# Kernel optimization log

Hardware: AMD Instinct MI355X
Metric: run time of the kernel (lower is better)

Reference implementation:

```python
import jax, jax.numpy as jnp
import numpy as np

N_HEADS = 16


def setup_inputs() -> dict:
    key = jax.random.key(0)
    k_x, k_len, k_pos, k_attn, k_proj = jax.random.split(key, 5)
    B, W, c, C = 4, 256, 32, 1024
    x = jax.random.normal(k_x, (B, W, c, C), dtype=jnp.float32)
    # ragged word lengths in [1, c]; left-aligned padding mask as in pad()
    lengths = jax.random.randint(k_len, (B, W), 1, c + 1)
    attention_mask = (jnp.arange(c)[None, None, :] < lengths[:, :, None]).astype(jnp.int32)
    pos_emb = jax.random.normal(k_pos, (W, C), dtype=jnp.float32) * 0.02
    attn_w = jax.random.normal(k_attn, (C, 3 * C), dtype=jnp.float32) * (C ** -0.5)
    proj_w = jax.random.normal(k_proj, (C, C), dtype=jnp.float32) * (C ** -0.5)
    return {"x": x, "attention_mask": attention_mask, "pos_emb": pos_emb,
            "attn_w": attn_w, "proj_w": proj_w}


def reference(x, attention_mask, pos_emb, attn_w, proj_w):
    # first_time=True path of CharAttention.forward (eval mode: dropout = identity)
    B, W, c, C = x.shape
    H = N_HEADS
    hd = C // H
    last_ix = jnp.sum(attention_mask, axis=2) - 1          # [B, W]

    qkv = jnp.einsum('bwce,ef->bwcf', x, attn_w)            # [B, W, c, 3C]
    q, k, v = jnp.split(qkv, 3, axis=-1)
    # [B, W, c, C] -> [B, W, H, c, hd]
    def to_heads(t):
        return t.reshape(B, W, c, H, hd).transpose(0, 1, 3, 2, 4)
    q, k, v = to_heads(q), to_heads(k), to_heads(v)

    scale = 1.0 / jnp.sqrt(jnp.asarray(hd, dtype=x.dtype))
    scores = jnp.einsum('bwhqd,bwhkd->bwhqk', q, k) * scale  # [B, W, H, c, c]
    causal = jnp.tril(jnp.ones((c, c), dtype=bool))
    scores = jnp.where(causal[None, None, None], scores, jnp.finfo(x.dtype).min)
    attn = jax.nn.softmax(scores, axis=-1)
    o = jnp.einsum('bwhqk,bwhkd->bwhqd', attn, v)            # [B, W, H, c, hd]
    o = o.transpose(0, 1, 3, 2, 4).reshape(B, W, c, C)       # [B, W, c, C]

    # gather the last real-character position of each word
    idx = last_ix[:, :, None, None]                          # [B, W, 1, 1]
    gathered = jnp.take_along_axis(o, idx, axis=2)[:, :, 0, :]  # [B, W, C]

    out = gathered + pos_emb[None, :, :]
    out = jnp.einsum('bwe,ef->bwf', out, proj_w)
    return out
```

## Files before the change

kernel.cpp:

```cpp
#include <hip/hip_runtime.h>
#include <hip/hip_bf16.h>
#include <stdint.h>

typedef __attribute__((ext_vector_type(8))) short short8;
typedef __attribute__((ext_vector_type(4))) float floatx4;

#define GPTR(p) (const __attribute__((address_space(1))) void*)(p)
#define LPTR(p) (__attribute__((address_space(3))) void*)(p)

__device__ __forceinline__ ushort f2bf(float f) {
    union { float f; uint32_t u; } v; v.f = f;
    uint32_t u = v.u;
    uint32_t r = (u + 0x7FFFu + ((u >> 16) & 1u)) >> 16;
    return (ushort)r;
}
__device__ __forceinline__ float bf2f(ushort b) {
    union { uint32_t u; float f; } v; v.u = ((uint32_t)b) << 16;
    return v.f;
}

__global__ void prep_kernel(const float* __restrict__ attn_w, const float* __restrict__ proj_w,
                            const float* __restrict__ x, const int* __restrict__ mask,
                            ushort* __restrict__ wqT, ushort* __restrict__ wk,
                            ushort* __restrict__ wvT, ushort* __restrict__ wpT,
                            ushort* __restrict__ xq) {
    __shared__ float tile[32][33];
    __shared__ int t_sh;
    const int bx = blockIdx.x, by = blockIdx.y;
    const int tid = threadIdx.x;

    if (bx >= 128) {
        int bw = (bx - 128) * 32 + by;
        if (tid < 32) {
            int s = mask[bw * 32 + tid];
            #pragma unroll
            for (int off = 16; off; off >>= 1) s += __shfl_xor(s, off);
            if (tid == 0) t_sh = s - 1;
        }
        __syncthreads();
        int t = t_sh;
        float4 v = ((const float4*)(x + ((size_t)bw * 32 + t) * 1024))[tid];
        ushort4 o;
        o.x = f2bf(v.x); o.y = f2bf(v.y); o.z = f2bf(v.z); o.w = f2bf(v.w);
        ((ushort4*)(xq + (size_t)bw * 1024))[tid] = o;
        return;
    }

    const int tx = tid & 31, ty = tid >> 5;
    const int r0 = by * 32;
    if (bx >= 96) {
        int c0 = (bx - 96) * 32;
        for (int i = ty; i < 32; i += 8)
            wk[(size_t)(r0 + i) * 1024 + c0 + tx] =
                f2bf(attn_w[(size_t)(r0 + i) * 3072 + 1024 + c0 + tx]);
        return;
    }
    const float* src; ushort* dst; int N, csrc0, c0;
    if (bx < 32)      { src = attn_w; dst = wqT; N = 3072; c0 = bx * 32;        csrc0 = c0; }
    else if (bx < 64) { src = attn_w; dst = wvT; N = 3072; c0 = (bx - 32) * 32; csrc0 = 2048 + c0; }
    else              { src = proj_w; dst = wpT; N = 1024; c0 = (bx - 64) * 32; csrc0 = c0; }
    for (int i = ty; i < 32; i += 8)
        tile[i][tx] = src[(size_t)(r0 + i) * N + csrc0 + tx];
    __syncthreads();
    for (int i = ty; i < 32; i += 8)
        dst[(size_t)(c0 + i) * 1024 + r0 + tx] = f2bf(tile[tx][i]);
}

template <bool OUT_BF16, bool ADD_POS>
__global__ __launch_bounds__(256)
void gemm64db_kernel(const ushort* __restrict__ A, int lda, long sA,
                     const ushort* __restrict__ Bt, int ldb, long sB,
                     void* __restrict__ C, int ldc, int cColPerZ, int K,
                     const float* __restrict__ pos) {
    __shared__ ushort As[2][64 * 32];
    __shared__ ushort Bs[2][64 * 32];

    const int bm = blockIdx.x, bn = blockIdx.y, z = blockIdx.z;
    A  += (size_t)z * sA;
    Bt += (size_t)z * sB;

    const int tid  = threadIdx.x;
    const int wave = tid >> 6;
    const int lane = tid & 63;
    const int wm = wave & 1, wn = wave >> 1;
    const int quad = lane >> 4, l15 = lane & 15;

    floatx4 acc[2][2] = {};

    const int srow = wave * 16 + (lane >> 2);
    const int kcol = (lane & 3) * 8;
    const ushort* gA = A  + (size_t)(bm * 64 + srow) * lda + kcol;
    const ushort* gB = Bt + (size_t)(bn * 64 + srow) * ldb + kcol;
    const int lofs = wave * 512;

    __builtin_amdgcn_global_load_lds(GPTR(gA), LPTR(As[0] + lofs), 16, 0, 0);
    __builtin_amdgcn_global_load_lds(GPTR(gB), LPTR(Bs[0] + lofs), 16, 0, 0);
    __syncthreads();

    int cur = 0;
    for (int kt = 0; kt < K; kt += 32) {
        if (kt + 32 < K) {
            __builtin_amdgcn_global_load_lds(GPTR(gA + kt + 32), LPTR(As[cur ^ 1] + lofs), 16, 0, 0);
            __builtin_amdgcn_global_load_lds(GPTR(gB + kt + 32), LPTR(Bs[cur ^ 1] + lofs), 16, 0, 0);
        }
        short8 af[2], bf[2];
        #pragma unroll
        for (int i = 0; i < 2; ++i)
            af[i] = *(const short8*)&As[cur][(wm * 32 + i * 16 + l15) * 32 + quad * 8];
        #pragma unroll
        for (int j = 0; j < 2; ++j)
            bf[j] = *(const short8*)&Bs[cur][(wn * 32 + j * 16 + l15) * 32 + quad * 8];
        #pragma unroll
        for (int i = 0; i < 2; ++i)
            #pragma unroll
            for (int j = 0; j < 2; ++j)
                acc[i][j] = __builtin_amdgcn_mfma_f32_16x16x32_bf16(af[i], bf[j], acc[i][j], 0, 0, 0);
        __syncthreads();
        cur ^= 1;
    }

    #pragma unroll
    for (int i = 0; i < 2; ++i) {
        #pragma unroll
        for (int j = 0; j < 2; ++j) {
            int r0 = bm * 64 + wm * 32 + i * 16 + quad * 4;
            int cc = z * cColPerZ + bn * 64 + wn * 32 + j * 16 + l15;
            #pragma unroll
            for (int r = 0; r < 4; ++r) {
                float v = acc[i][j][r];
                if (ADD_POS) v += pos[(size_t)((r0 + r) & 255) * 1024 + cc];
                size_t idx = (size_t)(r0 + r) * ldc + cc;
                if (OUT_BF16) ((ushort*)C)[idx] = f2bf(v);
                else          ((float*) C)[idx] = v;
            }
        }
    }
}

__global__ __launch_bounds__(256)
void gemmu_kernel(const ushort* __restrict__ A, const ushort* __restrict__ Bt,
                  ushort* __restrict__ C) {
    const int bm = blockIdx.x, bn = blockIdx.y, z = blockIdx.z;
    const int tid  = threadIdx.x;
    const int wave = tid >> 6;
    const int lane = tid & 63;
    const int wm = wave & 1, wn = wave >> 1;
    const int quad = lane >> 4, l15 = lane & 15;

    const ushort* Ab = A  + (size_t)(bm * 128 + wm * 64 + l15) * 1024 + z * 64 + quad * 8;
    const ushort* Bb = Bt + (size_t)(bn * 128 + wn * 64 + l15) * 1024 + z * 64 + quad * 8;

    short8 af[4][2], bfr[4][2];
    #pragma unroll
    for (int i = 0; i < 4; ++i)
        #pragma unroll
        for (int kk = 0; kk < 2; ++kk) {
            af[i][kk]  = *(const short8*)(Ab + (size_t)(i * 16) * 1024 + kk * 32);
            bfr[i][kk] = *(const short8*)(Bb + (size_t)(i * 16) * 1024 + kk * 32);
        }

    floatx4 acc[4][4] = {};
    #pragma unroll
    for (int kk = 0; kk < 2; ++kk)
        #pragma unroll
        for (int i = 0; i < 4; ++i)
            #pragma unroll
            for (int j = 0; j < 4; ++j)
                acc[i][j] = __builtin_amdgcn_mfma_f32_16x16x32_bf16(af[i][kk], bfr[j][kk], acc[i][j], 0, 0, 0);

    #pragma unroll
    for (int i = 0; i < 4; ++i) {
        #pragma unroll
        for (int j = 0; j < 4; ++j) {
            int r0 = bm * 128 + wm * 64 + i * 16 + quad * 4;
            int c  = bn * 128 + wn * 64 + j * 16 + l15;
            #pragma unroll
            for (int r = 0; r < 4; ++r)
                C[(size_t)(r0 + r) * 16384 + (size_t)z * 1024 + c] = f2bf(acc[i][j][r]);
        }
    }
}

__global__ __launch_bounds__(256)
void attn2_kernel(const float* __restrict__ x, const int* __restrict__ mask,
                  const ushort* __restrict__ U, ushort* __restrict__ Z) {
    __shared__ float  Sp[2][16][16];
    __shared__ float  Ss[16 * 36];
    __shared__ float  Ps[32 * 16];
    __shared__ int    t_sh;

    const int bw = blockIdx.x;
    const int tid = threadIdx.x;
    const int wave = tid >> 6, lane = tid & 63;
    const int quad = lane >> 4, l15 = lane & 15;

    if (tid < 32) {
        int s = mask[bw * 32 + tid];
        #pragma unroll
        for (int off = 16; off; off >>= 1) s += __shfl_xor(s, off);
        if (tid == 0) t_sh = s - 1;
    }
    __syncthreads();
    const int t = t_sh;

    const int m  = wave & 1;
    const int kh = wave >> 1;
    const int row = m * 16 + l15;
    const bool live = (row <= t);

    const float*  xrow = x + ((size_t)bw * 32 + row) * 1024 + kh * 512 + quad * 8;
    const ushort* urow = U + (size_t)bw * 16384 + (size_t)l15 * 1024 + kh * 512 + quad * 8;

    floatx4 acc = {0.f, 0.f, 0.f, 0.f};
    #pragma unroll
    for (int ks = 0; ks < 16; ++ks) {
        short8 a = (short8)0;
        if (live) {
            float4 v0 = *(const float4*)(xrow + ks * 32);
            float4 v1 = *(const float4*)(xrow + ks * 32 + 4);
            a[0] = (short)f2bf(v0.x); a[1] = (short)f2bf(v0.y);
            a[2] = (short)f2bf(v0.z); a[3] = (short)f2bf(v0.w);
            a[4] = (short)f2bf(v1.x); a[5] = (short)f2bf(v1.y);
            a[6] = (short)f2bf(v1.z); a[7] = (short)f2bf(v1.w);
        }
        short8 b = *(const short8*)(urow + ks * 32);
        acc = __builtin_amdgcn_mfma_f32_16x16x32_bf16(a, b, acc, 0, 0, 0);
    }

    if (kh == 1) {
        #pragma unroll
        for (int r = 0; r < 4; ++r) Sp[m][quad * 4 + r][l15] = acc[r];
    }
    __syncthreads();
    if (kh == 0) {
        #pragma unroll
        for (int r = 0; r < 4; ++r)
            Ss[l15 * 36 + m * 16 + quad * 4 + r] =
                (acc[r] + Sp[m][quad * 4 + r][l15]) * 0.125f;
    }
    __syncthreads();

    if (wave == 0) {
        float s[8]; float mx = -1e30f;
        #pragma unroll
        for (int r = 0; r < 8; ++r) {
            int j = quad * 8 + r;
            float v = Ss[l15 * 36 + j];
            v = (j <= t) ? v : -1e30f;
            s[r] = v; mx = fmaxf(mx, v);
        }
        mx = fmaxf(mx, __shfl_xor(mx, 16));
        mx = fmaxf(mx, __shfl_xor(mx, 32));
        float l = 0.f;
        #pragma unroll
        for (int r = 0; r < 8; ++r) { s[r] = __expf(s[r] - mx); l += s[r]; }
        l += __shfl_xor(l, 16);
        l += __shfl_xor(l, 32);
        float inv = 1.f / l;
        #pragma unroll
        for (int r = 0; r < 8; ++r)
            Ps[(quad * 8 + r) * 16 + l15] = s[r] * inv;
    }
    __syncthreads();

    const float4* xsrc = (const float4*)(x + (size_t)bw * 32768);
    float z[16][4];
    #pragma unroll
    for (int h = 0; h < 16; ++h)
        #pragma unroll
        for (int cc = 0; cc < 4; ++cc) z[h][cc] = 0.f;
    for (int j = 0; j <= t; ++j) {
        float4 p0 = *(const float4*)&Ps[j * 16 + 0];
        float4 p1 = *(const float4*)&Ps[j * 16 + 4];
        float4 p2 = *(const float4*)&Ps[j * 16 + 8];
        float4 p3 = *(const float4*)&Ps[j * 16 + 12];
        float pr[16] = {p0.x, p0.y, p0.z, p0.w, p1.x, p1.y, p1.z, p1.w,
                        p2.x, p2.y, p2.z, p2.w, p3.x, p3.y, p3.z, p3.w};
        float4 xv = xsrc[j * 256 + tid];
        float xf[4] = {xv.x, xv.y, xv.z, xv.w};
        #pragma unroll
        for (int h = 0; h < 16; ++h)
            #pragma unroll
            for (int cc = 0; cc < 4; ++cc)
                z[h][cc] += pr[h] * xf[cc];
    }
    const int e0 = tid * 4;
    #pragma unroll
    for (int h = 0; h < 16; ++h) {
        ushort4 o;
        o.x = f2bf(z[h][0]); o.y = f2bf(z[h][1]);
        o.z = f2bf(z[h][2]); o.w = f2bf(z[h][3]);
        *(ushort4*)&Z[(size_t)bw * 16384 + h * 1024 + e0] = o;
    }
}

extern "C" void kernel_launch(void* const* d_in, const int* in_sizes, int n_in,
                              void* d_out, int out_size, void* d_ws, size_t ws_size,
                              hipStream_t stream) {
    const float* x        = (const float*)d_in[0];
    const int*   mask     = (const int*)  d_in[1];
    const float* pos_emb  = (const float*)d_in[2];
    const float* attn_w   = (const float*)d_in[3];
    const float* proj_w   = (const float*)d_in[4];
    float*       out      = (float*)d_out;

    const long MB2 = 1048576;

    char* ws = (char*)d_ws;
    size_t off = 0;
    ushort* U_bf  = (ushort*)(ws + off); off += (size_t)16 * MB2 * 2;
    ushort* Z_bf  = (ushort*)(ws + off); off += (size_t)16 * MB2 * 2;
    ushort* wqT   = (ushort*)(ws + off); off += MB2 * 2;
    ushort* wk    = (ushort*)(ws + off); off += MB2 * 2;
    ushort* wvT   = (ushort*)(ws + off); off += MB2 * 2;
    ushort* wpT   = (ushort*)(ws + off); off += MB2 * 2;
    ushort* xq_bf = (ushort*)(ws + off); off += MB2 * 2;
    ushort* q_bf  = (ushort*)(ws + off); off += MB2 * 2;
    ushort* y_bf  = (ushort*)(ws + off); off += MB2 * 2;

    prep_kernel<<<dim3(160, 32), 256, 0, stream>>>(attn_w, proj_w, x, mask,
                                                   wqT, wk, wvT, wpT, xq_bf);

    gemm64db_kernel<true, false><<<dim3(16, 16, 1), 256, 0, stream>>>(
        xq_bf, 1024, 0, wqT, 1024, 0, (void*)q_bf, 1024, 0, 1024, nullptr);

    gemmu_kernel<<<dim3(8, 8, 16), 256, 0, stream>>>(q_bf, wk, U_bf);

    attn2_kernel<<<1024, 256, 0, stream>>>(x, mask, U_bf, Z_bf);

    gemm64db_kernel<true, true><<<dim3(16, 1, 16), 256, 0, stream>>>(
        Z_bf, 16384, 1024, wvT, 1024, 65536, (void*)y_bf, 1024, 64, 1024, pos_emb);

    gemm64db_kernel<false, false><<<dim3(16, 16, 1), 256, 0, stream>>>(
        y_bf, 1024, 0, wpT, 1024, 0, (void*)out, 1024, 0, 1024, nullptr);
}
```

Measured before the change: 277.8 us.

## Fuse all six stage kernels into one persistent kernel with grid barriers

Replaces the six separate launches (weight prep, q GEMM, U GEMM, attention, V GEMM, proj GEMM) with one persistent kernel of 512 blocks. The blocks loop over each stage's tiles and meet at an atomic-based grid barrier between stages. The aim is to remove per-launch overhead and the idle gaps between dependent kernels. In exchange, the barrier has a timeout break that could silently let blocks proceed early. It also depends on all 512 blocks being co-resident (launch bounds of 2 blocks per CU), and the fixed grid may balance uneven stages worse than the original launches.

```diff
diff --git a/kernel.cpp b/kernel.cpp
--- a/kernel.cpp
+++ b/kernel.cpp
@@ -14,19 +14,37 @@
     uint32_t r = (u + 0x7FFFu + ((u >> 16) & 1u)) >> 16;
     return (ushort)r;
 }
-__device__ __forceinline__ float bf2f(ushort b) {
-    union { uint32_t u; float f; } v; v.u = ((uint32_t)b) << 16;
-    return v.f;
-}
-
-__global__ void prep_kernel(const float* __restrict__ attn_w, const float* __restrict__ proj_w,
+
+__device__ int g_bar_count;
+__device__ int g_bar_gen;
+
+__device__ __forceinline__ void grid_sync(int nb) {
+    __syncthreads();
+    if (threadIdx.x == 0) {
+        int g = __hip_atomic_load(&g_bar_gen, __ATOMIC_RELAXED, __HIP_MEMORY_SCOPE_AGENT);
+        int prev = __hip_atomic_fetch_add(&g_bar_count, 1, __ATOMIC_ACQ_REL, __HIP_MEMORY_SCOPE_AGENT);
+        if (prev == nb - 1) {
+            __hip_atomic_store(&g_bar_count, 0, __ATOMIC_RELAXED, __HIP_MEMORY_SCOPE_AGENT);
+            __hip_atomic_store(&g_bar_gen, g + 1, __ATOMIC_RELEASE, __HIP_MEMORY_SCOPE_AGENT);
+        } else {
+            long long t0 = clock64();
+            while (__hip_atomic_load(&g_bar_gen, __ATOMIC_ACQUIRE, __HIP_MEMORY_SCOPE_AGENT) == g) {
+                __builtin_amdgcn_s_sleep(8);
+                if (clock64() - t0 > 100000000LL) break;
+            }
+        }
+    }
+    __syncthreads();
+}
+
+__device__ __forceinline__ void prep_body(int bx, int by,
+                            const float* __restrict__ attn_w, const float* __restrict__ proj_w,
                             const float* __restrict__ x, const int* __restrict__ mask,
                             ushort* __restrict__ wqT, ushort* __restrict__ wk,
                             ushort* __restrict__ wvT, ushort* __restrict__ wpT,
                             ushort* __restrict__ xq) {
     __shared__ float tile[32][33];
-    __shared__ int t_sh;
-    const int bx = blockIdx.x, by = blockIdx.y;
+    __shared__ int t_sh0;
     const int tid = threadIdx.x;
 
     if (bx >= 128) {
@@ -35,14 +53,15 @@
             int s = mask[bw * 32 + tid];
             #pragma unroll
             for (int off = 16; off; off >>= 1) s += __shfl_xor(s, off);
-            if (tid == 0) t_sh = s - 1;
+            if (tid == 0) t_sh0 = s - 1;
         }
         __syncthreads();
-        int t = t_sh;
+        int t = t_sh0;
         float4 v = ((const float4*)(x + ((size_t)bw * 32 + t) * 1024))[tid];
         ushort4 o;
         o.x = f2bf(v.x); o.y = f2bf(v.y); o.z = f2bf(v.z); o.w = f2bf(v.w);
         ((ushort4*)(xq + (size_t)bw * 1024))[tid] = o;
+        __syncthreads();
         return;
     }
 
@@ -64,18 +83,17 @@
     __syncthreads();
     for (int i = ty; i < 32; i += 8)
         dst[(size_t)(c0 + i) * 1024 + r0 + tx] = f2bf(tile[tx][i]);
+    __syncthreads();
 }
 
 template <bool OUT_BF16, bool ADD_POS>
-__global__ __launch_bounds__(256)
-void gemm64db_kernel(const ushort* __restrict__ A, int lda, long sA,
+__device__ __forceinline__ void gemm_body(const ushort* __restrict__ A, int lda, long sA,
                      const ushort* __restrict__ Bt, int ldb, long sB,
                      void* __restrict__ C, int ldc, int cColPerZ, int K,
-                     const float* __restrict__ pos) {
+                     const float* __restrict__ pos, int bm, int bn, int z) {
     __shared__ ushort As[2][64 * 32];
     __shared__ ushort Bs[2][64 * 32];
 
-    const int bm = blockIdx.x, bn = blockIdx.y, z = blockIdx.z;
     A  += (size_t)z * sA;
     Bt += (size_t)z * sB;
 
@@ -137,10 +155,8 @@
     }
 }
 
-__global__ __launch_bounds__(256)
-void gemmu_kernel(const ushort* __restrict__ A, const ushort* __restrict__ Bt,
-                  ushort* __restrict__ C) {
-    const int bm = blockIdx.x, bn = blockIdx.y, z = blockIdx.z;
+__device__ __forceinline__ void gemmu_body(const ushort* __restrict__ A, const ushort* __restrict__ Bt,
+                  ushort* __restrict__ C, int bm, int bn, int z) {
     const int tid  = threadIdx.x;
     const int wave = tid >> 6;
     const int lane = tid & 63;
@@ -181,15 +197,13 @@
     }
 }
 
-__global__ __launch_bounds__(256)
-void attn2_kernel(const float* __restrict__ x, const int* __restrict__ mask,
-                  const ushort* __restrict__ U, ushort* __restrict__ Z) {
+__device__ __forceinline__ void attn2_body(const float* __restrict__ x, const int* __restrict__ mask,
+                  const ushort* __restrict__ U, ushort* __restrict__ Zo, int bw) {
     __shared__ float  Sp[2][16][16];
     __shared__ float  Ss[16 * 36];
     __shared__ float  Ps[32 * 16];
     __shared__ int    t_sh;
 
-    const int bw = blockIdx.x;
     const int tid = threadIdx.x;
     const int wave = tid >> 6, lane = tid & 63;
     const int quad = lane >> 4, l15 = lane & 15;
@@ -264,11 +278,11 @@
     __syncthreads();
 
     const float4* xsrc = (const float4*)(x + (size_t)bw * 32768);
-    float z[16][4];
+    float zz[16][4];
     #pragma unroll
     for (int h = 0; h < 16; ++h)
         #pragma unroll
-        for (int cc = 0; cc < 4; ++cc) z[h][cc] = 0.f;
+        for (int cc = 0; cc < 4; ++cc) zz[h][cc] = 0.f;
     for (int j = 0; j <= t; ++j) {
         float4 p0 = *(const float4*)&Ps[j * 16 + 0];
         float4 p1 = *(const float4*)&Ps[j * 16 + 4];
@@ -282,16 +296,54 @@
         for (int h = 0; h < 16; ++h)
             #pragma unroll
             for (int cc = 0; cc < 4; ++cc)
-                z[h][cc] += pr[h] * xf[cc];
+                zz[h][cc] += pr[h] * xf[cc];
     }
     const int e0 = tid * 4;
     #pragma unroll
     for (int h = 0; h < 16; ++h) {
         ushort4 o;
-        o.x = f2bf(z[h][0]); o.y = f2bf(z[h][1]);
-        o.z = f2bf(z[h][2]); o.w = f2bf(z[h][3]);
-        *(ushort4*)&Z[(size_t)bw * 16384 + h * 1024 + e0] = o;
-    }
+        o.x = f2bf(zz[h][0]); o.y = f2bf(zz[h][1]);
+        o.z = f2bf(zz[h][2]); o.w = f2bf(zz[h][3]);
+        *(ushort4*)&Zo[(size_t)bw * 16384 + h * 1024 + e0] = o;
+    }
+}
+
+__global__ __launch_bounds__(256, 2)
+void mega_kernel(const float* __restrict__ x, const int* __restrict__ mask,
+                 const float* __restrict__ pos, const float* __restrict__ attn_w,
+                 const float* __restrict__ proj_w, float* __restrict__ out,
+                 ushort* __restrict__ U, ushort* __restrict__ Z,
+                 ushort* __restrict__ wqT, ushort* __restrict__ wk,
+                 ushort* __restrict__ wvT, ushort* __restrict__ wpT,
+                 ushort* __restrict__ xq, ushort* __restrict__ q,
+                 ushort* __restrict__ y) {
+    const int nb = gridDim.x;
+
+    for (int task = blockIdx.x; task < 5120; task += nb)
+        prep_body(task % 160, task / 160, attn_w, proj_w, x, mask, wqT, wk, wvT, wpT, xq);
+    grid_sync(nb);
+
+    for (int task = blockIdx.x; task < 256; task += nb)
+        gemm_body<true, false>(xq, 1024, 0, wqT, 1024, 0, (void*)q, 1024, 0, 1024,
+                               nullptr, task & 15, task >> 4, 0);
+    grid_sync(nb);
+
+    for (int task = blockIdx.x; task < 1024; task += nb)
+        gemmu_body(q, wk, U, task & 7, (task >> 3) & 7, task >> 6);
+    grid_sync(nb);
+
+    for (int task = blockIdx.x; task < 1024; task += nb)
+        attn2_body(x, mask, U, Z, task);
+    grid_sync(nb);
+
+    for (int task = blockIdx.x; task < 256; task += nb)
+        gemm_body<true, true>(Z, 16384, 1024, wvT, 1024, 65536, (void*)y, 1024, 64, 1024,
+                              pos, task & 15, 0, task >> 4);
+    grid_sync(nb);
+
+    for (int task = blockIdx.x; task < 256; task += nb)
+        gemm_body<false, false>(y, 1024, 0, wpT, 1024, 0, (void*)out, 1024, 0, 1024,
+                                nullptr, task & 15, task >> 4, 0);
 }
 
 extern "C" void kernel_launch(void* const* d_in, const int* in_sizes, int n_in,
@@ -318,19 +370,7 @@
     ushort* q_bf  = (ushort*)(ws + off); off += MB2 * 2;
     ushort* y_bf  = (ushort*)(ws + off); off += MB2 * 2;
 
-    prep_kernel<<<dim3(160, 32), 256, 0, stream>>>(attn_w, proj_w, x, mask,
-                                                   wqT, wk, wvT, wpT, xq_bf);
-
-    gemm64db_kernel<true, false><<<dim3(16, 16, 1), 256, 0, stream>>>(
-        xq_bf, 1024, 0, wqT, 1024, 0, (void*)q_bf, 1024, 0, 1024, nullptr);
-
-    gemmu_kernel<<<dim3(8, 8, 16), 256, 0, stream>>>(q_bf, wk, U_bf);
-
-    attn2_kernel<<<1024, 256, 0, stream>>>(x, mask, U_bf, Z_bf);
-
-    gemm64db_kernel<true, true><<<dim3(16, 1, 16), 256, 0, stream>>>(
-        Z_bf, 16384, 1024, wvT, 1024, 65536, (void*)y_bf, 1024, 64, 1024, pos_emb);
-
-    gemm64db_kernel<false, false><<<dim3(16, 16, 1), 256, 0, stream>>>(
-        y_bf, 1024, 0, wpT, 1024, 0, (void*)out, 1024, 0, 1024, nullptr);
-}
+    mega_kernel<<<dim3(512), dim3(256), 0, stream>>>(
+        x, mask, pos_emb, attn_w, proj_w, out,
+        U_bf, Z_bf, wqT, wk, wvT, wpT, xq_bf, q_bf, y_bf);
+}
```

Result: slower. 789.8 us (+184.3%).

## Split K across two wave groups in small GEMMs with LDS reduction

Applied to the files above, without the earlier changes.

The 64x64-tile GEMM kernel now runs 8 waves per block, with two groups of four waves each handling half of the K dimension in separate double-buffered LDS slices. After the loop, the second group writes its partial accumulators to a shared float buffer and the first group adds them before the epilogue. This doubles waves per block for these small-grid GEMMs (256 blocks) to hide latency and halves the serial K loop. The cost is extra LDS use, one extra reduction pass and a barrier.

```diff
diff --git a/kernel.cpp b/kernel.cpp
--- a/kernel.cpp
+++ b/kernel.cpp
@@ -13,10 +13,6 @@
     uint32_t u = v.u;
     uint32_t r = (u + 0x7FFFu + ((u >> 16) & 1u)) >> 16;
     return (ushort)r;
-}
-__device__ __forceinline__ float bf2f(ushort b) {
-    union { uint32_t u; float f; } v; v.u = ((uint32_t)b) << 16;
-    return v.f;
 }
 
 __global__ void prep_kernel(const float* __restrict__ attn_w, const float* __restrict__ proj_w,
@@ -67,49 +63,55 @@
 }
 
 template <bool OUT_BF16, bool ADD_POS>
-__global__ __launch_bounds__(256)
-void gemm64db_kernel(const ushort* __restrict__ A, int lda, long sA,
+__global__ __launch_bounds__(512)
+void gemm64x8_kernel(const ushort* __restrict__ A, int lda, long sA,
                      const ushort* __restrict__ Bt, int ldb, long sB,
                      void* __restrict__ C, int ldc, int cColPerZ, int K,
                      const float* __restrict__ pos) {
-    __shared__ ushort As[2][64 * 32];
-    __shared__ ushort Bs[2][64 * 32];
+    __shared__ ushort As[2][2][64 * 32];
+    __shared__ ushort Bs[2][2][64 * 32];
+    __shared__ float  Cred[64 * 64];
 
     const int bm = blockIdx.x, bn = blockIdx.y, z = blockIdx.z;
     A  += (size_t)z * sA;
     Bt += (size_t)z * sB;
 
     const int tid  = threadIdx.x;
-    const int wave = tid >> 6;
+    const int w    = tid >> 6;
     const int lane = tid & 63;
-    const int wm = wave & 1, wn = wave >> 1;
+    const int kh   = w >> 2;
+    const int wq   = w & 3;
+    const int wm = wq & 1, wn = wq >> 1;
     const int quad = lane >> 4, l15 = lane & 15;
 
     floatx4 acc[2][2] = {};
 
-    const int srow = wave * 16 + (lane >> 2);
-    const int kcol = (lane & 3) * 8;
-    const ushort* gA = A  + (size_t)(bm * 64 + srow) * lda + kcol;
-    const ushort* gB = Bt + (size_t)(bn * 64 + srow) * ldb + kcol;
-    const int lofs = wave * 512;
-
-    __builtin_amdgcn_global_load_lds(GPTR(gA), LPTR(As[0] + lofs), 16, 0, 0);
-    __builtin_amdgcn_global_load_lds(GPTR(gB), LPTR(Bs[0] + lofs), 16, 0, 0);
+    const int KH = K >> 1;
+    const int srow = wq * 16 + (lane >> 2);
+    const int scol = kh * KH + (lane & 3) * 8;
+    const ushort* gA = A  + (size_t)(bm * 64 + srow) * lda + scol;
+    const ushort* gB = Bt + (size_t)(bn * 64 + srow) * ldb + scol;
+    const int lofs = wq * 512;
+
+    __builtin_amdgcn_global_load_lds(GPTR(gA), LPTR(As[0][kh] + lofs), 16, 0, 0);
+    __builtin_amdgcn_global_load_lds(GPTR(gB), LPTR(Bs[0][kh] + lofs), 16, 0, 0);
     __syncthreads();
 
     int cur = 0;
-    for (int kt = 0; kt < K; kt += 32) {
-        if (kt + 32 < K) {
-            __builtin_amdgcn_global_load_lds(GPTR(gA + kt + 32), LPTR(As[cur ^ 1] + lofs), 16, 0, 0);
-            __builtin_amdgcn_global_load_lds(GPTR(gB + kt + 32), LPTR(Bs[cur ^ 1] + lofs), 16, 0, 0);
+    const int NS = KH >> 5;
+    for (int s = 0; s < NS; ++s) {
+        if (s + 1 < NS) {
+            int kt = (s + 1) * 32;
+            __builtin_amdgcn_global_load_lds(GPTR(gA + kt), LPTR(As[cur ^ 1][kh] + lofs), 16, 0, 0);
+            __builtin_amdgcn_global_load_lds(GPTR(gB + kt), LPTR(Bs[cur ^ 1][kh] + lofs), 16, 0, 0);
         }
         short8 af[2], bf[2];
         #pragma unroll
         for (int i = 0; i < 2; ++i)
-            af[i] = *(const short8*)&As[cur][(wm * 32 + i * 16 + l15) * 32 + quad * 8];
+            af[i] = *(const short8*)&As[cur][kh][(wm * 32 + i * 16 + l15) * 32 + quad * 8];
         #pragma unroll
         for (int j = 0; j < 2; ++j)
-            bf[j] = *(const short8*)&Bs[cur][(wn * 32 + j * 16 + l15) * 32 + quad * 8];
+            bf[j] = *(const short8*)&Bs[cur][kh][(wn * 32 + j * 16 + l15) * 32 + quad * 8];
         #pragma unroll
         for (int i = 0; i < 2; ++i)
             #pragma unroll
@@ -119,19 +121,34 @@
         cur ^= 1;
     }
 
-    #pragma unroll
-    for (int i = 0; i < 2; ++i) {
-        #pragma unroll
-        for (int j = 0; j < 2; ++j) {
-            int r0 = bm * 64 + wm * 32 + i * 16 + quad * 4;
-            int cc = z * cColPerZ + bn * 64 + wn * 32 + j * 16 + l15;
-            #pragma unroll
-            for (int r = 0; r < 4; ++r) {
-                float v = acc[i][j][r];
-                if (ADD_POS) v += pos[(size_t)((r0 + r) & 255) * 1024 + cc];
-                size_t idx = (size_t)(r0 + r) * ldc + cc;
-                if (OUT_BF16) ((ushort*)C)[idx] = f2bf(v);
-                else          ((float*) C)[idx] = v;
+    if (kh == 1) {
+        #pragma unroll
+        for (int i = 0; i < 2; ++i)
+            #pragma unroll
+            for (int j = 0; j < 2; ++j)
+                #pragma unroll
+                for (int r = 0; r < 4; ++r)
+                    Cred[(wm * 32 + i * 16 + quad * 4 + r) * 64 + wn * 32 + j * 16 + l15] =
+                        acc[i][j][r];
+    }
+    __syncthreads();
+    if (kh == 0) {
+        #pragma unroll
+        for (int i = 0; i < 2; ++i) {
+            #pragma unroll
+            for (int j = 0; j < 2; ++j) {
+                int lr = wm * 32 + i * 16 + quad * 4;
+                int lc = wn * 32 + j * 16 + l15;
+                int r0 = bm * 64 + lr;
+                int cc = z * cColPerZ + bn * 64 + lc;
+                #pragma unroll
+                for (int r = 0; r < 4; ++r) {
+                    float v = acc[i][j][r] + Cred[(lr + r) * 64 + lc];
+                    if (ADD_POS) v += pos[(size_t)((r0 + r) & 255) * 1024 + cc];
+                    size_t idx = (size_t)(r0 + r) * ldc + cc;
+                    if (OUT_BF16) ((ushort*)C)[idx] = f2bf(v);
+                    else          ((float*) C)[idx] = v;
+                }
             }
         }
     }
@@ -321,16 +338,16 @@
     prep_kernel<<<dim3(160, 32), 256, 0, stream>>>(attn_w, proj_w, x, mask,
                                                    wqT, wk, wvT, wpT, xq_bf);
 
-    gemm64db_kernel<true, false><<<dim3(16, 16, 1), 256, 0, stream>>>(
+    gemm64x8_kernel<true, false><<<dim3(16, 16, 1), 512, 0, stream>>>(
         xq_bf, 1024, 0, wqT, 1024, 0, (void*)q_bf, 1024, 0, 1024, nullptr);
 
     gemmu_kernel<<<dim3(8, 8, 16), 256, 0, stream>>>(q_bf, wk, U_bf);
 
     attn2_kernel<<<1024, 256, 0, stream>>>(x, mask, U_bf, Z_bf);
 
-    gemm64db_kernel<true, true><<<dim3(16, 1, 16), 256, 0, stream>>>(
+    gemm64x8_kernel<true, true><<<dim3(16, 1, 16), 512, 0, stream>>>(
         Z_bf, 16384, 1024, wvT, 1024, 65536, (void*)y_bf, 1024, 64, 1024, pos_emb);
 
-    gemm64db_kernel<false, false><<<dim3(16, 16, 1), 256, 0, stream>>>(
+    gemm64x8_kernel<false, false><<<dim3(16, 16, 1), 512, 0, stream>>>(
         y_bf, 1024, 0, wpT, 1024, 0, (void*)out, 1024, 0, 1024, nullptr);
 }
```

After: 269.5 us. 3.0% less time.
